# Kernel tuning notes

Hardware: AMD Instinct MI355X
Metric: run time of the kernel (lower is better)

Reference implementation:

```python
import jax, jax.numpy as jnp
import numpy as np

# Dropout layers are treated as identity (eval mode) for a deterministic reference.

def _branch(x, Ws):
    # pattern in original: relu -> (dropout) -> linear, repeated; last linear has no trailing relu
    for W in Ws:
        x = jax.nn.relu(x) @ W.T
    return x

def _cross_mul(s, e):
    # z[k,h] = sum_j s[k,h]*e[k,j] = s[k,h] * sum_j e[k,j]
    return s * jnp.sum(e, axis=-1, keepdims=True)

def setup_inputs() -> dict:
    key = jax.random.key(0)
    ks = jax.random.split(key, 12)
    def lin(k, out_d, in_d):
        return jax.random.normal(k, (out_d, in_d), dtype=jnp.float32) * (1.0 / np.sqrt(in_d))
    B = 65536
    return {
        "result": jax.random.normal(ks[0], (B, 4, 768), dtype=jnp.float32),
        "sW1": lin(ks[1], 96, 768), "sW2": lin(ks[2], 48, 96), "sW3": lin(ks[3], 24, 48),
        "sW4": lin(ks[4], 12, 24), "sW5": lin(ks[5], 2, 12),
        "eW1": lin(ks[6], 96, 768), "eW2": lin(ks[7], 48, 96), "eW3": lin(ks[8], 24, 48),
        "eW4": lin(ks[9], 12, 24), "eW5": lin(ks[10], 8, 12),
        "s_seq": jnp.array([0.25, 0.25, 0.25, 0.25], dtype=jnp.float32),
        "s_pair": jnp.array([0.5, 0.5], dtype=jnp.float32),
        "e_seq": jnp.array([0.25, 0.25, 0.25, 0.25], dtype=jnp.float32),
        "e_pair": jnp.array([0.5, 0.5], dtype=jnp.float32),
        "cross_w": jnp.array([0.5, 0.5], dtype=jnp.float32),
    }

def reference(result, sW1, sW2, sW3, sW4, sW5, eW1, eW2, eW3, eW4, eW5,
              s_seq, s_pair, e_seq, e_pair, cross_w):
    sWs = (sW1, sW2, sW3, sW4, sW5)
    eWs = (eW1, eW2, eW3, eW4, eW5)
    # soft attention pools over the 4 "token" slots
    pair_e = result[:, 0, :] * e_pair[0] + result[:, 2, :] * e_pair[1]
    pair_s = result[:, 0, :] * s_pair[0] + result[:, 2, :] * s_pair[1]
    seq_e = jnp.einsum('bsd,s->bd', result, e_seq)
    seq_s = jnp.einsum('bsd,s->bd', result, s_seq)
    pair_e_out = _branch(pair_e, eWs)  # [B, 8]
    pair_s_out = _branch(pair_s, sWs)  # [B, 2]
    seq_e_out = _branch(seq_e, eWs)    # [B, 8]
    seq_s_out = _branch(seq_s, sWs)    # [B, 2]
    pair_cross = _cross_mul(pair_s_out, pair_e_out)
    seq_cross = _cross_mul(seq_s_out, seq_e_out)
    return cross_w[0] * pair_cross + cross_w[1] * seq_cross
```

## Files before the change

kernel.cpp:

```cpp
#include <hip/hip_runtime.h>

typedef _Float16 half8 __attribute__((ext_vector_type(8)));
typedef _Float16 half4v __attribute__((ext_vector_type(4)));
typedef float floatx4 __attribute__((ext_vector_type(4)));

#define MFMA16(a, b, c) __builtin_amdgcn_mfma_f32_16x16x32_f16((a), (b), (c), 0, 0, 0)

#define OFF_W1 0
#define OFF_W2 147456
#define OFF_W3 156672
#define OFF_W4 160768
#define OFF_W5 161792

__global__ __launch_bounds__(64) void prep_weights(
    const float* __restrict__ eW1, const float* __restrict__ sW1,
    const float* __restrict__ eW2, const float* __restrict__ sW2,
    const float* __restrict__ eW3, const float* __restrict__ sW3,
    const float* __restrict__ eW4, const float* __restrict__ sW4,
    const float* __restrict__ eW5, const float* __restrict__ sW5,
    _Float16* __restrict__ ws)
{
    int b = blockIdx.x;
    int lane = threadIdx.x;
    const float* src;
    _Float16* dst;
    int N, K, nt, ks;
    if (b < 288) {
        int mat = b / 144, r = b % 144;
        nt = r / 24; ks = r % 24;
        src = mat ? sW1 : eW1; N = 96; K = 768;
        dst = ws + OFF_W1 + (size_t)((mat * 6 + nt) * 24 + ks) * 512;
    } else if (b < 306) {
        int i = b - 288, mat = i / 9, r = i % 9;
        nt = r / 3; ks = r % 3;
        src = mat ? sW2 : eW2; N = 48; K = 96;
        dst = ws + OFF_W2 + (size_t)((mat * 3 + nt) * 3 + ks) * 512;
    } else if (b < 314) {
        int i = b - 306, mat = i / 4, r = i % 4;
        nt = r / 2; ks = r % 2;
        src = mat ? sW3 : eW3; N = 24; K = 48;
        dst = ws + OFF_W3 + (size_t)((mat * 2 + nt) * 2 + ks) * 512;
    } else if (b < 316) {
        int mat = b - 314;
        nt = 0; ks = 0;
        src = mat ? sW4 : eW4; N = 12; K = 24;
        dst = ws + OFF_W4 + (size_t)mat * 512;
    } else {
        int mat = b - 316;
        nt = 0; ks = 0;
        src = mat ? sW5 : eW5; N = mat ? 2 : 8; K = 12;
        dst = ws + OFF_W5 + (size_t)mat * 512;
    }
    int n = nt * 16 + (lane & 15);
    int kb = ks * 32 + (lane >> 4) * 8;
    for (int j = 0; j < 8; ++j) {
        int k = kb + j;
        float v = (n < N && k < K) ? src[n * K + k] : 0.0f;
        dst[lane * 8 + j] = (_Float16)v;
    }
}

__global__ __launch_bounds__(256) void fused_net(
    const float* __restrict__ result,
    const float* __restrict__ e_pair, const float* __restrict__ s_pair,
    const float* __restrict__ e_seq,  const float* __restrict__ s_seq,
    const float* __restrict__ cross_w,
    const _Float16* __restrict__ ws,
    float* __restrict__ out)
{
    __shared__ __align__(16) unsigned char lds_raw[18432 + 26624 + 2048 + 512];
    _Float16* bufA = (_Float16*)lds_raw;
    _Float16* bufB = (_Float16*)(lds_raw + 18432);
    float* EoLDS = (float*)(lds_raw + 18432 + 26624);
    float* SoLDS = (float*)(lds_raw + 18432 + 26624 + 2048);

    const int tid  = threadIdx.x;
    const int lane = tid & 63;
    const int wave = tid >> 6;
    const int l15  = lane & 15;
    const int q    = lane >> 4;
    const int mat  = wave >> 1;
    const int mh   = wave & 1;
    const int sbase = blockIdx.x * 32;

    const float ep0 = e_pair[0], ep1 = e_pair[1];
    const float sp0 = s_pair[0], sp1 = s_pair[1];
    const float es0 = e_seq[0], es1 = e_seq[1], es2 = e_seq[2], es3 = e_seq[3];
    const float ss0 = s_seq[0], ss1 = s_seq[1], ss2 = s_seq[2], ss3 = s_seq[3];

    const floatx4 zf4 = {0.f, 0.f, 0.f, 0.f};

    floatx4 acc[2][6];
#pragma unroll
    for (int m = 0; m < 2; ++m)
#pragma unroll
        for (int n = 0; n < 6; ++n) acc[m][n] = zf4;

    const int kq = tid & 15;
    const int sg = tid >> 4;
    _Float16* Am = bufA + mat * 4608;
    const half8* Bw1 = (const half8*)(ws + OFF_W1) + (size_t)mat * 6 * 24 * 64;

    for (int c = 0; c < 12; ++c) {
#pragma unroll
        for (int pass = 0; pass < 2; ++pass) {
            int s = pass * 16 + sg;
            const float4* rp = (const float4*)(result + (size_t)(sbase + s) * 3072 + c * 64);
            float4 r0 = rp[kq];
            float4 r1 = rp[kq + 192];
            float4 r2 = rp[kq + 384];
            float4 r3 = rp[kq + 576];

            float pex = fmaxf(ep0 * r0.x + ep1 * r2.x, 0.f);
            float pey = fmaxf(ep0 * r0.y + ep1 * r2.y, 0.f);
            float pez = fmaxf(ep0 * r0.z + ep1 * r2.z, 0.f);
            float pew = fmaxf(ep0 * r0.w + ep1 * r2.w, 0.f);
            float psx = fmaxf(sp0 * r0.x + sp1 * r2.x, 0.f);
            float psy = fmaxf(sp0 * r0.y + sp1 * r2.y, 0.f);
            float psz = fmaxf(sp0 * r0.z + sp1 * r2.z, 0.f);
            float psw = fmaxf(sp0 * r0.w + sp1 * r2.w, 0.f);
            float sex = fmaxf(es0 * r0.x + es1 * r1.x + es2 * r2.x + es3 * r3.x, 0.f);
            float sey = fmaxf(es0 * r0.y + es1 * r1.y + es2 * r2.y + es3 * r3.y, 0.f);
            float sez = fmaxf(es0 * r0.z + es1 * r1.z + es2 * r2.z + es3 * r3.z, 0.f);
            float sew = fmaxf(es0 * r0.w + es1 * r1.w + es2 * r2.w + es3 * r3.w, 0.f);
            float ssx = fmaxf(ss0 * r0.x + ss1 * r1.x + ss2 * r2.x + ss3 * r3.x, 0.f);
            float ssy = fmaxf(ss0 * r0.y + ss1 * r1.y + ss2 * r2.y + ss3 * r3.y, 0.f);
            float ssz = fmaxf(ss0 * r0.z + ss1 * r1.z + ss2 * r2.z + ss3 * r3.z, 0.f);
            float ssw = fmaxf(ss0 * r0.w + ss1 * r1.w + ss2 * r2.w + ss3 * r3.w, 0.f);

            half4v hpe = {(_Float16)pex, (_Float16)pey, (_Float16)pez, (_Float16)pew};
            half4v hps = {(_Float16)psx, (_Float16)psy, (_Float16)psz, (_Float16)psw};
            half4v hse = {(_Float16)sex, (_Float16)sey, (_Float16)sez, (_Float16)sew};
            half4v hss = {(_Float16)ssx, (_Float16)ssy, (_Float16)ssz, (_Float16)ssw};

            int co = kq * 4;
            *(half4v*)(bufA + s * 72 + co)               = hpe;
            *(half4v*)(bufA + (32 + s) * 72 + co)        = hse;
            *(half4v*)(bufA + 4608 + s * 72 + co)        = hps;
            *(half4v*)(bufA + 4608 + (32 + s) * 72 + co) = hss;
        }
        __syncthreads();

#pragma unroll
        for (int ks2 = 0; ks2 < 2; ++ks2) {
            int kg = c * 2 + ks2;
            half8 a0 = *(const half8*)(Am + (mh * 32 + l15) * 72 + ks2 * 32 + q * 8);
            half8 a1 = *(const half8*)(Am + (mh * 32 + 16 + l15) * 72 + ks2 * 32 + q * 8);
#pragma unroll
            for (int nt = 0; nt < 6; ++nt) {
                half8 b = Bw1[(nt * 24 + kg) * 64 + lane];
                acc[0][nt] = MFMA16(a0, b, acc[0][nt]);
                acc[1][nt] = MFMA16(a1, b, acc[1][nt]);
            }
        }
        __syncthreads();
    }

    _Float16* Y1h = bufB;
#pragma unroll
    for (int m = 0; m < 2; ++m)
#pragma unroll
        for (int nt = 0; nt < 6; ++nt)
#pragma unroll
            for (int r = 0; r < 4; ++r) {
                int row = mat * 64 + mh * 32 + m * 16 + q * 4 + r;
                Y1h[row * 104 + nt * 16 + l15] = (_Float16)fmaxf(acc[m][nt][r], 0.f);
            }
    __syncthreads();

    floatx4 acc2[2][3];
#pragma unroll
    for (int m = 0; m < 2; ++m)
#pragma unroll
        for (int n = 0; n < 3; ++n) acc2[m][n] = zf4;
    {
        const _Float16* A2 = Y1h + mat * 64 * 104;
        const half8* Bw2 = (const half8*)(ws + OFF_W2) + (size_t)mat * 3 * 3 * 64;
#pragma unroll
        for (int ks2 = 0; ks2 < 3; ++ks2) {
            half8 a0 = *(const half8*)(A2 + (mh * 32 + l15) * 104 + ks2 * 32 + q * 8);
            half8 a1 = *(const half8*)(A2 + (mh * 32 + 16 + l15) * 104 + ks2 * 32 + q * 8);
#pragma unroll
            for (int nt = 0; nt < 3; ++nt) {
                half8 b = Bw2[(nt * 3 + ks2) * 64 + lane];
                acc2[0][nt] = MFMA16(a0, b, acc2[0][nt]);
                acc2[1][nt] = MFMA16(a1, b, acc2[1][nt]);
            }
        }
    }
    _Float16* Y2h = bufA;
#pragma unroll
    for (int m = 0; m < 2; ++m)
#pragma unroll
        for (int nt = 0; nt < 3; ++nt)
#pragma unroll
            for (int r = 0; r < 4; ++r) {
                int row = mat * 64 + mh * 32 + m * 16 + q * 4 + r;
                Y2h[row * 72 + nt * 16 + l15] = (_Float16)fmaxf(acc2[m][nt][r], 0.f);
            }
    for (int i = tid; i < 2048; i += 256) {
        int row = i >> 4;
        Y2h[row * 72 + 48 + (i & 15)] = (_Float16)0.f;
    }
    __syncthreads();

    floatx4 acc3[2][2];
#pragma unroll
    for (int m = 0; m < 2; ++m)
#pragma unroll
        for (int n = 0; n < 2; ++n) acc3[m][n] = zf4;
    {
        const _Float16* A3 = bufA + mat * 64 * 72;
        const half8* Bw3 = (const half8*)(ws + OFF_W3) + (size_t)mat * 2 * 2 * 64;
#pragma unroll
        for (int ks2 = 0; ks2 < 2; ++ks2) {
            half8 a0 = *(const half8*)(A3 + (mh * 32 + l15) * 72 + ks2 * 32 + q * 8);
            half8 a1 = *(const half8*)(A3 + (mh * 32 + 16 + l15) * 72 + ks2 * 32 + q * 8);
#pragma unroll
            for (int nt = 0; nt < 2; ++nt) {
                half8 b = Bw3[(nt * 2 + ks2) * 64 + lane];
                acc3[0][nt] = MFMA16(a0, b, acc3[0][nt]);
                acc3[1][nt] = MFMA16(a1, b, acc3[1][nt]);
            }
        }
    }
    _Float16* Y3h = bufB;
#pragma unroll
    for (int m = 0; m < 2; ++m)
#pragma unroll
        for (int nt = 0; nt < 2; ++nt)
#pragma unroll
            for (int r = 0; r < 4; ++r) {
                int row = mat * 64 + mh * 32 + m * 16 + q * 4 + r;
                Y3h[row * 40 + nt * 16 + l15] = (_Float16)fmaxf(acc3[m][nt][r], 0.f);
            }
    __syncthreads();

    floatx4 acc4[2];
    {
        const _Float16* A4 = bufB + mat * 64 * 40;
        const half8* Bw4 = (const half8*)(ws + OFF_W4) + (size_t)mat * 64;
        half8 a0 = *(const half8*)(A4 + (mh * 32 + l15) * 40 + q * 8);
        half8 a1 = *(const half8*)(A4 + (mh * 32 + 16 + l15) * 40 + q * 8);
        half8 b = Bw4[lane];
        acc4[0] = MFMA16(a0, b, zf4);
        acc4[1] = MFMA16(a1, b, zf4);
    }
    _Float16* Y4h = bufA;
#pragma unroll
    for (int m = 0; m < 2; ++m)
#pragma unroll
        for (int r = 0; r < 4; ++r) {
            int row = mat * 64 + mh * 32 + m * 16 + q * 4 + r;
            Y4h[row * 40 + l15] = (_Float16)fmaxf(acc4[m][r], 0.f);
        }
    for (int i = tid; i < 2048; i += 256) {
        int row = i >> 4;
        Y4h[row * 40 + 16 + (i & 15)] = (_Float16)0.f;
    }
    __syncthreads();

    floatx4 acc5[2];
    {
        const _Float16* A5 = bufA + mat * 64 * 40;
        const half8* Bw5 = (const half8*)(ws + OFF_W5) + (size_t)mat * 64;
        half8 a0 = *(const half8*)(A5 + (mh * 32 + l15) * 40 + q * 8);
        half8 a1 = *(const half8*)(A5 + (mh * 32 + 16 + l15) * 40 + q * 8);
        half8 b = Bw5[lane];
        acc5[0] = MFMA16(a0, b, zf4);
        acc5[1] = MFMA16(a1, b, zf4);
    }
    if (mat == 0) {
        if (l15 < 8) {
#pragma unroll
            for (int m = 0; m < 2; ++m)
#pragma unroll
                for (int r = 0; r < 4; ++r) {
                    int row = mh * 32 + m * 16 + q * 4 + r;
                    EoLDS[row * 8 + l15] = acc5[m][r];
                }
        }
    } else {
        if (l15 < 2) {
#pragma unroll
            for (int m = 0; m < 2; ++m)
#pragma unroll
                for (int r = 0; r < 4; ++r) {
                    int row = mh * 32 + m * 16 + q * 4 + r;
                    SoLDS[row * 2 + l15] = acc5[m][r];
                }
        }
    }
    __syncthreads();

    if (tid < 64) {
        int sample = tid >> 1;
        int h = tid & 1;
        float cw0 = cross_w[0], cw1 = cross_w[1];
        float pes = 0.f, ses = 0.f;
#pragma unroll
        for (int j = 0; j < 8; ++j) {
            pes += EoLDS[sample * 8 + j];
            ses += EoLDS[(32 + sample) * 8 + j];
        }
        float v = cw0 * SoLDS[sample * 2 + h] * pes
                + cw1 * SoLDS[(32 + sample) * 2 + h] * ses;
        out[(size_t)(sbase + sample) * 2 + h] = v;
    }
}

extern "C" void kernel_launch(void* const* d_in, const int* in_sizes, int n_in,
                              void* d_out, int out_size, void* d_ws, size_t ws_size,
                              hipStream_t stream) {
    (void)n_in; (void)out_size; (void)ws_size;
    const float* result = (const float*)d_in[0];
    const float* sW1 = (const float*)d_in[1];
    const float* sW2 = (const float*)d_in[2];
    const float* sW3 = (const float*)d_in[3];
    const float* sW4 = (const float*)d_in[4];
    const float* sW5 = (const float*)d_in[5];
    const float* eW1 = (const float*)d_in[6];
    const float* eW2 = (const float*)d_in[7];
    const float* eW3 = (const float*)d_in[8];
    const float* eW4 = (const float*)d_in[9];
    const float* eW5 = (const float*)d_in[10];
    const float* s_seq  = (const float*)d_in[11];
    const float* s_pair = (const float*)d_in[12];
    const float* e_seq  = (const float*)d_in[13];
    const float* e_pair = (const float*)d_in[14];
    const float* cross_w = (const float*)d_in[15];
    _Float16* ws = (_Float16*)d_ws;
    float* out = (float*)d_out;

    int B = in_sizes[0] / 3072;

    prep_weights<<<dim3(318), dim3(64), 0, stream>>>(
        eW1, sW1, eW2, sW2, eW3, sW3, eW4, sW4, eW5, sW5, ws);

    fused_net<<<dim3(B / 32), dim3(256), 0, stream>>>(
        result, e_pair, s_pair, e_seq, s_seq, cross_w, ws, out);
}
```

Before: 1.061 ms.

## Double-buffer input via async global-to-LDS loads and pool inside MFMA fragment build

Replaces the synchronous per-chunk global loads plus pooled-fp16 LDS staging with direct global_load_lds async copies of raw fp32 input into a double-buffered LDS region. Each wave then computes its own pooling (pair or seq) while building MFMA A-fragments from the raw data, and the next chunk's copy overlaps with the current MFMAs. LDS is reduced and shared across layers with extra barriers, and the launch bound now requests 4 blocks per CU to raise occupancy. The trade-off is redundant pooling arithmetic across waves and more LDS reads of fp32 data.

```diff
diff --git a/kernel.cpp b/kernel.cpp
--- a/kernel.cpp
+++ b/kernel.cpp
@@ -1,7 +1,6 @@
 #include <hip/hip_runtime.h>
 
 typedef _Float16 half8 __attribute__((ext_vector_type(8)));
-typedef _Float16 half4v __attribute__((ext_vector_type(4)));
 typedef float floatx4 __attribute__((ext_vector_type(4)));
 
 #define MFMA16(a, b, c) __builtin_amdgcn_mfma_f32_16x16x32_f16((a), (b), (c), 0, 0, 0)
@@ -11,6 +10,13 @@
 #define OFF_W3 156672
 #define OFF_W4 160768
 #define OFF_W5 161792
+
+typedef __attribute__((address_space(3))) unsigned int lds_uint;
+typedef __attribute__((address_space(1))) unsigned int glob_uint;
+
+__device__ __forceinline__ void async_copy16(const void* g, void* l) {
+    __builtin_amdgcn_global_load_lds((const glob_uint*)g, (lds_uint*)l, 16, 0, 0);
+}
 
 __global__ __launch_bounds__(64) void prep_weights(
     const float* __restrict__ eW1, const float* __restrict__ sW1,
@@ -60,7 +66,51 @@
     }
 }
 
-__global__ __launch_bounds__(256) void fused_net(
+__device__ __forceinline__ const float4* rawp(const unsigned char* buf, int s, int t, int k16) {
+    return (const float4*)(buf + ((s >> 1) * 1040 + ((s & 1) << 9) + (((t << 3) | k16) << 4)));
+}
+
+__device__ __forceinline__ half8 frag_pair(const unsigned char* buf, int s, int q,
+                                           float w0, float w1) {
+    float4 a0 = *rawp(buf, s, 0, 2 * q);
+    float4 a1 = *rawp(buf, s, 0, 2 * q + 1);
+    float4 c0 = *rawp(buf, s, 2, 2 * q);
+    float4 c1 = *rawp(buf, s, 2, 2 * q + 1);
+    half8 h;
+    h[0] = (_Float16)fmaxf(w0 * a0.x + w1 * c0.x, 0.f);
+    h[1] = (_Float16)fmaxf(w0 * a0.y + w1 * c0.y, 0.f);
+    h[2] = (_Float16)fmaxf(w0 * a0.z + w1 * c0.z, 0.f);
+    h[3] = (_Float16)fmaxf(w0 * a0.w + w1 * c0.w, 0.f);
+    h[4] = (_Float16)fmaxf(w0 * a1.x + w1 * c1.x, 0.f);
+    h[5] = (_Float16)fmaxf(w0 * a1.y + w1 * c1.y, 0.f);
+    h[6] = (_Float16)fmaxf(w0 * a1.z + w1 * c1.z, 0.f);
+    h[7] = (_Float16)fmaxf(w0 * a1.w + w1 * c1.w, 0.f);
+    return h;
+}
+
+__device__ __forceinline__ half8 frag_seq(const unsigned char* buf, int s, int q,
+                                          float w0, float w1, float w2, float w3) {
+    float4 a0 = *rawp(buf, s, 0, 2 * q);
+    float4 a1 = *rawp(buf, s, 0, 2 * q + 1);
+    float4 b0 = *rawp(buf, s, 1, 2 * q);
+    float4 b1 = *rawp(buf, s, 1, 2 * q + 1);
+    float4 c0 = *rawp(buf, s, 2, 2 * q);
+    float4 c1 = *rawp(buf, s, 2, 2 * q + 1);
+    float4 d0 = *rawp(buf, s, 3, 2 * q);
+    float4 d1 = *rawp(buf, s, 3, 2 * q + 1);
+    half8 h;
+    h[0] = (_Float16)fmaxf(w0 * a0.x + w1 * b0.x + w2 * c0.x + w3 * d0.x, 0.f);
+    h[1] = (_Float16)fmaxf(w0 * a0.y + w1 * b0.y + w2 * c0.y + w3 * d0.y, 0.f);
+    h[2] = (_Float16)fmaxf(w0 * a0.z + w1 * b0.z + w2 * c0.z + w3 * d0.z, 0.f);
+    h[3] = (_Float16)fmaxf(w0 * a0.w + w1 * b0.w + w2 * c0.w + w3 * d0.w, 0.f);
+    h[4] = (_Float16)fmaxf(w0 * a1.x + w1 * b1.x + w2 * c1.x + w3 * d1.x, 0.f);
+    h[5] = (_Float16)fmaxf(w0 * a1.y + w1 * b1.y + w2 * c1.y + w3 * d1.y, 0.f);
+    h[6] = (_Float16)fmaxf(w0 * a1.z + w1 * b1.z + w2 * c1.z + w3 * d1.z, 0.f);
+    h[7] = (_Float16)fmaxf(w0 * a1.w + w1 * b1.w + w2 * c1.w + w3 * d1.w, 0.f);
+    return h;
+}
+
+__global__ __launch_bounds__(256, 4) void fused_net(
     const float* __restrict__ result,
     const float* __restrict__ e_pair, const float* __restrict__ s_pair,
     const float* __restrict__ e_seq,  const float* __restrict__ s_seq,
@@ -68,11 +118,9 @@
     const _Float16* __restrict__ ws,
     float* __restrict__ out)
 {
-    __shared__ __align__(16) unsigned char lds_raw[18432 + 26624 + 2048 + 512];
-    _Float16* bufA = (_Float16*)lds_raw;
-    _Float16* bufB = (_Float16*)(lds_raw + 18432);
-    float* EoLDS = (float*)(lds_raw + 18432 + 26624);
-    float* SoLDS = (float*)(lds_raw + 18432 + 26624 + 2048);
+    __shared__ __align__(16) unsigned char lds_raw[35840];
+    float* EoLDS = (float*)(lds_raw + 33280);
+    float* SoLDS = (float*)(lds_raw + 33280 + 2048);
 
     const int tid  = threadIdx.x;
     const int lane = tid & 63;
@@ -83,80 +131,76 @@
     const int mh   = wave & 1;
     const int sbase = blockIdx.x * 32;
 
-    const float ep0 = e_pair[0], ep1 = e_pair[1];
-    const float sp0 = s_pair[0], sp1 = s_pair[1];
-    const float es0 = e_seq[0], es1 = e_seq[1], es2 = e_seq[2], es3 = e_seq[3];
-    const float ss0 = s_seq[0], ss1 = s_seq[1], ss2 = s_seq[2], ss3 = s_seq[3];
+    float w0, w1, w2 = 0.f, w3 = 0.f;
+    if (mh == 0) {
+        w0 = mat ? s_pair[0] : e_pair[0];
+        w1 = mat ? s_pair[1] : e_pair[1];
+    } else {
+        w0 = mat ? s_seq[0] : e_seq[0];
+        w1 = mat ? s_seq[1] : e_seq[1];
+        w2 = mat ? s_seq[2] : e_seq[2];
+        w3 = mat ? s_seq[3] : e_seq[3];
+    }
 
     const floatx4 zf4 = {0.f, 0.f, 0.f, 0.f};
 
+    const int dma_so  = lane >> 5;
+    const int dma_u   = lane & 31;
+    const int dma_t   = dma_u >> 3;
+    const int dma_k16 = dma_u & 7;
+    const size_t dma_goff = (size_t)(dma_t * 768 + dma_k16 * 4);
+
     floatx4 acc[2][6];
 #pragma unroll
     for (int m = 0; m < 2; ++m)
 #pragma unroll
         for (int n = 0; n < 6; ++n) acc[m][n] = zf4;
 
-    const int kq = tid & 15;
-    const int sg = tid >> 4;
-    _Float16* Am = bufA + mat * 4608;
-    const half8* Bw1 = (const half8*)(ws + OFF_W1) + (size_t)mat * 6 * 24 * 64;
-
-    for (int c = 0; c < 12; ++c) {
-#pragma unroll
-        for (int pass = 0; pass < 2; ++pass) {
-            int s = pass * 16 + sg;
-            const float4* rp = (const float4*)(result + (size_t)(sbase + s) * 3072 + c * 64);
-            float4 r0 = rp[kq];
-            float4 r1 = rp[kq + 192];
-            float4 r2 = rp[kq + 384];
-            float4 r3 = rp[kq + 576];
-
-            float pex = fmaxf(ep0 * r0.x + ep1 * r2.x, 0.f);
-            float pey = fmaxf(ep0 * r0.y + ep1 * r2.y, 0.f);
-            float pez = fmaxf(ep0 * r0.z + ep1 * r2.z, 0.f);
-            float pew = fmaxf(ep0 * r0.w + ep1 * r2.w, 0.f);
-            float psx = fmaxf(sp0 * r0.x + sp1 * r2.x, 0.f);
-            float psy = fmaxf(sp0 * r0.y + sp1 * r2.y, 0.f);
-            float psz = fmaxf(sp0 * r0.z + sp1 * r2.z, 0.f);
-            float psw = fmaxf(sp0 * r0.w + sp1 * r2.w, 0.f);
-            float sex = fmaxf(es0 * r0.x + es1 * r1.x + es2 * r2.x + es3 * r3.x, 0.f);
-            float sey = fmaxf(es0 * r0.y + es1 * r1.y + es2 * r2.y + es3 * r3.y, 0.f);
-            float sez = fmaxf(es0 * r0.z + es1 * r1.z + es2 * r2.z + es3 * r3.z, 0.f);
-            float sew = fmaxf(es0 * r0.w + es1 * r1.w + es2 * r2.w + es3 * r3.w, 0.f);
-            float ssx = fmaxf(ss0 * r0.x + ss1 * r1.x + ss2 * r2.x + ss3 * r3.x, 0.f);
-            float ssy = fmaxf(ss0 * r0.y + ss1 * r1.y + ss2 * r2.y + ss3 * r3.y, 0.f);
-            float ssz = fmaxf(ss0 * r0.z + ss1 * r1.z + ss2 * r2.z + ss3 * r3.z, 0.f);
-            float ssw = fmaxf(ss0 * r0.w + ss1 * r1.w + ss2 * r2.w + ss3 * r3.w, 0.f);
-
-            half4v hpe = {(_Float16)pex, (_Float16)pey, (_Float16)pez, (_Float16)pew};
-            half4v hps = {(_Float16)psx, (_Float16)psy, (_Float16)psz, (_Float16)psw};
-            half4v hse = {(_Float16)sex, (_Float16)sey, (_Float16)sez, (_Float16)sew};
-            half4v hss = {(_Float16)ssx, (_Float16)ssy, (_Float16)ssz, (_Float16)ssw};
-
-            int co = kq * 4;
-            *(half4v*)(bufA + s * 72 + co)               = hpe;
-            *(half4v*)(bufA + (32 + s) * 72 + co)        = hse;
-            *(half4v*)(bufA + 4608 + s * 72 + co)        = hps;
-            *(half4v*)(bufA + 4608 + (32 + s) * 72 + co) = hss;
+    const half8* Bw1 = (const half8*)(ws + OFF_W1) + (size_t)mat * (6 * 24 * 64);
+
+    {
+        const float* gbase = result + (size_t)sbase * 3072;
+#pragma unroll
+        for (int i = 0; i < 4; ++i) {
+            int blk = wave * 4 + i;
+            const float* g = gbase + (size_t)(2 * blk + dma_so) * 3072 + dma_goff;
+            async_copy16(g, lds_raw + blk * 1040);
+        }
+    }
+    __syncthreads();
+
+#pragma unroll 2
+    for (int c = 0; c < 24; ++c) {
+        const unsigned char* cur = lds_raw + (c & 1) * 16640;
+        unsigned char* nxt = lds_raw + ((c + 1) & 1) * 16640;
+        if (c < 23) {
+            const float* gbase = result + (size_t)sbase * 3072 + (c + 1) * 32;
+#pragma unroll
+            for (int i = 0; i < 4; ++i) {
+                int blk = wave * 4 + i;
+                const float* g = gbase + (size_t)(2 * blk + dma_so) * 3072 + dma_goff;
+                async_copy16(g, nxt + blk * 1040);
+            }
+        }
+        half8 a0f, a1f;
+        if (mh == 0) {
+            a0f = frag_pair(cur, l15,      q, w0, w1);
+            a1f = frag_pair(cur, l15 + 16, q, w0, w1);
+        } else {
+            a0f = frag_seq(cur, l15,      q, w0, w1, w2, w3);
+            a1f = frag_seq(cur, l15 + 16, q, w0, w1, w2, w3);
+        }
+#pragma unroll
+        for (int nt = 0; nt < 6; ++nt) {
+            half8 bf = Bw1[(nt * 24 + c) * 64 + lane];
+            acc[0][nt] = MFMA16(a0f, bf, acc[0][nt]);
+            acc[1][nt] = MFMA16(a1f, bf, acc[1][nt]);
         }
         __syncthreads();
-
-#pragma unroll
-        for (int ks2 = 0; ks2 < 2; ++ks2) {
-            int kg = c * 2 + ks2;
-            half8 a0 = *(const half8*)(Am + (mh * 32 + l15) * 72 + ks2 * 32 + q * 8);
-            half8 a1 = *(const half8*)(Am + (mh * 32 + 16 + l15) * 72 + ks2 * 32 + q * 8);
-#pragma unroll
-            for (int nt = 0; nt < 6; ++nt) {
-                half8 b = Bw1[(nt * 24 + kg) * 64 + lane];
-                acc[0][nt] = MFMA16(a0, b, acc[0][nt]);
-                acc[1][nt] = MFMA16(a1, b, acc[1][nt]);
-            }
-        }
-        __syncthreads();
-    }
-
-    _Float16* Y1h = bufB;
+    }
+
+    _Float16* Y = (_Float16*)lds_raw;
+
 #pragma unroll
     for (int m = 0; m < 2; ++m)
 #pragma unroll
@@ -164,7 +208,7 @@
 #pragma unroll
             for (int r = 0; r < 4; ++r) {
                 int row = mat * 64 + mh * 32 + m * 16 + q * 4 + r;
-                Y1h[row * 104 + nt * 16 + l15] = (_Float16)fmaxf(acc[m][nt][r], 0.f);
+                Y[row * 104 + nt * 16 + l15] = (_Float16)fmaxf(acc[m][nt][r], 0.f);
             }
     __syncthreads();
 
@@ -174,21 +218,21 @@
 #pragma unroll
         for (int n = 0; n < 3; ++n) acc2[m][n] = zf4;
     {
-        const _Float16* A2 = Y1h + mat * 64 * 104;
-        const half8* Bw2 = (const half8*)(ws + OFF_W2) + (size_t)mat * 3 * 3 * 64;
+        const _Float16* A2 = Y + mat * 64 * 104;
+        const half8* Bw2 = (const half8*)(ws + OFF_W2) + (size_t)mat * (3 * 3 * 64);
 #pragma unroll
         for (int ks2 = 0; ks2 < 3; ++ks2) {
             half8 a0 = *(const half8*)(A2 + (mh * 32 + l15) * 104 + ks2 * 32 + q * 8);
             half8 a1 = *(const half8*)(A2 + (mh * 32 + 16 + l15) * 104 + ks2 * 32 + q * 8);
 #pragma unroll
             for (int nt = 0; nt < 3; ++nt) {
-                half8 b = Bw2[(nt * 3 + ks2) * 64 + lane];
-                acc2[0][nt] = MFMA16(a0, b, acc2[0][nt]);
-                acc2[1][nt] = MFMA16(a1, b, acc2[1][nt]);
-            }
-        }
-    }
-    _Float16* Y2h = bufA;
+                half8 bf = Bw2[(nt * 3 + ks2) * 64 + lane];
+                acc2[0][nt] = MFMA16(a0, bf, acc2[0][nt]);
+                acc2[1][nt] = MFMA16(a1, bf, acc2[1][nt]);
+            }
+        }
+    }
+    __syncthreads();
 #pragma unroll
     for (int m = 0; m < 2; ++m)
 #pragma unroll
@@ -196,11 +240,11 @@
 #pragma unroll
             for (int r = 0; r < 4; ++r) {
                 int row = mat * 64 + mh * 32 + m * 16 + q * 4 + r;
-                Y2h[row * 72 + nt * 16 + l15] = (_Float16)fmaxf(acc2[m][nt][r], 0.f);
+                Y[row * 72 + nt * 16 + l15] = (_Float16)fmaxf(acc2[m][nt][r], 0.f);
             }
     for (int i = tid; i < 2048; i += 256) {
         int row = i >> 4;
-        Y2h[row * 72 + 48 + (i & 15)] = (_Float16)0.f;
+        Y[row * 72 + 48 + (i & 15)] = (_Float16)0.f;
     }
     __syncthreads();
 
@@ -210,21 +254,21 @@
 #pragma unroll
         for (int n = 0; n < 2; ++n) acc3[m][n] = zf4;
     {
-        const _Float16* A3 = bufA + mat * 64 * 72;
-        const half8* Bw3 = (const half8*)(ws + OFF_W3) + (size_t)mat * 2 * 2 * 64;
+        const _Float16* A3 = Y + mat * 64 * 72;
+        const half8* Bw3 = (const half8*)(ws + OFF_W3) + (size_t)mat * (2 * 2 * 64);
 #pragma unroll
         for (int ks2 = 0; ks2 < 2; ++ks2) {
             half8 a0 = *(const half8*)(A3 + (mh * 32 + l15) * 72 + ks2 * 32 + q * 8);
             half8 a1 = *(const half8*)(A3 + (mh * 32 + 16 + l15) * 72 + ks2 * 32 + q * 8);
 #pragma unroll
             for (int nt = 0; nt < 2; ++nt) {
-                half8 b = Bw3[(nt * 2 + ks2) * 64 + lane];
-                acc3[0][nt] = MFMA16(a0, b, acc3[0][nt]);
-                acc3[1][nt] = MFMA16(a1, b, acc3[1][nt]);
-            }
-        }
-    }
-    _Float16* Y3h = bufB;
+                half8 bf = Bw3[(nt * 2 + ks2) * 64 + lane];
+                acc3[0][nt] = MFMA16(a0, bf, acc3[0][nt]);
+                acc3[1][nt] = MFMA16(a1, bf, acc3[1][nt]);
+            }
+        }
+    }
+    __syncthreads();
 #pragma unroll
     for (int m = 0; m < 2; ++m)
 #pragma unroll
@@ -232,43 +276,47 @@
 #pragma unroll
             for (int r = 0; r < 4; ++r) {
                 int row = mat * 64 + mh * 32 + m * 16 + q * 4 + r;
-                Y3h[row * 40 + nt * 16 + l15] = (_Float16)fmaxf(acc3[m][nt][r], 0.f);
-            }
+                Y[row * 40 + nt * 16 + l15] = (_Float16)fmaxf(acc3[m][nt][r], 0.f);
+            }
+    for (int i = tid; i < 1024; i += 256) {
+        int row = i >> 3;
+        Y[row * 40 + 24 + (i & 7)] = (_Float16)0.f;
+    }
     __syncthreads();
 
     floatx4 acc4[2];
     {
-        const _Float16* A4 = bufB + mat * 64 * 40;
+        const _Float16* A4 = Y + mat * 64 * 40;
         const half8* Bw4 = (const half8*)(ws + OFF_W4) + (size_t)mat * 64;
         half8 a0 = *(const half8*)(A4 + (mh * 32 + l15) * 40 + q * 8);
         half8 a1 = *(const half8*)(A4 + (mh * 32 + 16 + l15) * 40 + q * 8);
-        half8 b = Bw4[lane];
-        acc4[0] = MFMA16(a0, b, zf4);
-        acc4[1] = MFMA16(a1, b, zf4);
-    }
-    _Float16* Y4h = bufA;
+        half8 bf = Bw4[lane];
+        acc4[0] = MFMA16(a0, bf, zf4);
+        acc4[1] = MFMA16(a1, bf, zf4);
+    }
+    __syncthreads();
 #pragma unroll
     for (int m = 0; m < 2; ++m)
 #pragma unroll
         for (int r = 0; r < 4; ++r) {
             int row = mat * 64 + mh * 32 + m * 16 + q * 4 + r;
-            Y4h[row * 40 + l15] = (_Float16)fmaxf(acc4[m][r], 0.f);
-        }
-    for (int i = tid; i < 2048; i += 256) {
-        int row = i >> 4;
-        Y4h[row * 40 + 16 + (i & 15)] = (_Float16)0.f;
+            Y[row * 40 + l15] = (_Float16)fmaxf(acc4[m][r], 0.f);
+        }
+    for (int i = tid; i < 2560; i += 256) {
+        int row = i / 20;
+        Y[row * 40 + 12 + (i % 20)] = (_Float16)0.f;
     }
     __syncthreads();
 
     floatx4 acc5[2];
     {
-        const _Float16* A5 = bufA + mat * 64 * 40;
+        const _Float16* A5 = Y + mat * 64 * 40;
         const half8* Bw5 = (const half8*)(ws + OFF_W5) + (size_t)mat * 64;
         half8 a0 = *(const half8*)(A5 + (mh * 32 + l15) * 40 + q * 8);
         half8 a1 = *(const half8*)(A5 + (mh * 32 + 16 + l15) * 40 + q * 8);
-        half8 b = Bw5[lane];
-        acc5[0] = MFMA16(a0, b, zf4);
-        acc5[1] = MFMA16(a1, b, zf4);
+        half8 bf = Bw5[lane];
+        acc5[0] = MFMA16(a0, bf, zf4);
+        acc5[1] = MFMA16(a1, bf, zf4);
     }
     if (mat == 0) {
         if (l15 < 8) {
```

Result: no change. 1.061 ms (-0.1%).
